# Kernel optimization log

Hardware: AMD Instinct MI355X
Metric: run time of the kernel (lower is better)

## Reference

```python
import jax, jax.numpy as jnp
import numpy as np

NUM_HEADS = 12
EPS = 1e-5


def setup_inputs() -> dict:
    key = jax.random.key(0)
    k0, k1, k2 = jax.random.split(key, 3)
    B, C, D = 2, 768, 14  # batch, hidden_size, img_size//16
    x = jax.random.normal(k0, (B, C, D, D, D), dtype=jnp.float32)
    norm_w = jnp.ones((C,), dtype=jnp.float32)
    norm_b = jnp.zeros((C,), dtype=jnp.float32)
    qkv_w = jax.random.normal(k1, (3 * C, C), dtype=jnp.float32) * 0.02
    out_w = jax.random.normal(k2, (C, C), dtype=jnp.float32) * 0.02
    out_b = jnp.zeros((C,), dtype=jnp.float32)
    return {"x": x, "norm_w": norm_w, "norm_b": norm_b,
            "qkv_w": qkv_w, "out_w": out_w, "out_b": out_b}


def reference(x, norm_w, norm_b, qkv_w, out_w, out_b):
    B, C, D, H, W = x.shape
    nh = NUM_HEADS
    dh = C // nh
    scale = dh ** -0.5

    # b c d h w -> b (d h w) c
    t = jnp.transpose(x, (0, 2, 3, 4, 1)).reshape(B, D * H * W, C)
    N = t.shape[1]

    # LayerNorm over channel dim
    mu = jnp.mean(t, axis=-1, keepdims=True)
    var = jnp.mean(jnp.square(t - mu), axis=-1, keepdims=True)
    tn = (t - mu) / jnp.sqrt(var + EPS) * norm_w + norm_b

    # qkv projection (no bias), split as (3, heads, dim_head)
    qkv = tn @ qkv_w.T                       # [B, N, 3C]
    qkv = qkv.reshape(B, N, 3, nh, dh)
    qkv = jnp.transpose(qkv, (2, 0, 3, 1, 4))  # [3, B, nh, N, dh]
    q, k, v = qkv[0], qkv[1], qkv[2]

    att = jax.nn.softmax(jnp.einsum('blxn,blyn->blxy', q, k) * scale, axis=-1)
    out = jnp.einsum('blxy,blyn->blxn', att, v)  # [B, nh, N, dh]

    out = jnp.transpose(out, (0, 2, 1, 3)).reshape(B, N, C)
    out = out @ out_w.T + out_b

    out = out.reshape(B, D, H, W, C)
    out = jnp.transpose(out, (0, 4, 1, 2, 3))  # b d h w c -> b c d h w
    return out + x
```

## Files before the change

### kernel.cpp

```cpp
#include <hip/hip_runtime.h>

typedef unsigned short u16;
typedef unsigned int u32;

#define SPA 2744
#define CH  768
#define NH  12
#define DH  64
#define BB  2
#define TC  2304
#define MTOT (BB*SPA)
#define CVTB 2304

typedef __bf16 bf16x8_t __attribute__((ext_vector_type(8)));
typedef __bf16 bf16x4_t __attribute__((ext_vector_type(4)));
typedef short  s16x4    __attribute__((ext_vector_type(4)));
typedef float  f32x4_t  __attribute__((ext_vector_type(4)));

static __device__ __forceinline__ u16 f2bf(float f) {
    union { float f; u32 u; } v; v.f = f;
    u32 u = v.u;
    u += 0x7fffu + ((u >> 16) & 1u);
    return (u16)(u >> 16);
}

static __device__ __forceinline__ void gld16(const u16* g, u16* l) {
    __builtin_amdgcn_global_load_lds(
        (const __attribute__((address_space(1))) u32*)(size_t)g,
        (__attribute__((address_space(3))) u32*)(u32)(size_t)l, 16, 0, 0);
}

__global__ __launch_bounds__(256) void cvtln_kernel(const float* __restrict__ qkv_w,
                                                    u16* __restrict__ qkvw_bf, int n4a,
                                                    const float* __restrict__ out_w,
                                                    u16* __restrict__ outw_bf,
                                                    const float* __restrict__ x,
                                                    const float* __restrict__ w,
                                                    const float* __restrict__ bta,
                                                    u16* __restrict__ tn) {
    int tid = threadIdx.x;
    if (blockIdx.x < CVTB) {
        int i = blockIdx.x * 256 + tid;
        const float* src; u16* dst; int idx;
        if (i < n4a) { src = qkv_w; dst = qkvw_bf; idx = i; }
        else { src = out_w; dst = outw_bf; idx = i - n4a; }
        float4 f = ((const float4*)src)[idx];
        uint2 o;
        o.x = (u32)f2bf(f.x) | ((u32)f2bf(f.y) << 16);
        o.y = (u32)f2bf(f.z) | ((u32)f2bf(f.w) << 16);
        ((uint2*)dst)[idx] = o;
        return;
    }
    int bid = blockIdx.x - CVTB;
    __shared__ f32x4_t redS[4][16];
    __shared__ f32x4_t redQ[4][16];
    __shared__ u16 T[32][68];
    int grp = tid & 15, chl = tid >> 4;
    int wvi = tid >> 6, l16g = tid & 15;
    (void)l16g;
    int tok0 = bid * 64 + grp * 4;
    int gb = (tok0 + 3 < MTOT) ? tok0 : (MTOT - 4);
    int b = gb / SPA, n = gb - b * SPA;
    const float* base = x + (size_t)b * CH * SPA + n;

    f32x4_t s4 = {0.f, 0.f, 0.f, 0.f}, q4 = {0.f, 0.f, 0.f, 0.f};
    for (int c0 = 0; c0 < CH; c0 += 16) {
        float4 v = *(const float4*)(base + (size_t)(c0 + chl) * SPA);
        s4[0] += v.x; s4[1] += v.y; s4[2] += v.z; s4[3] += v.w;
        q4[0] += v.x * v.x; q4[1] += v.y * v.y; q4[2] += v.z * v.z; q4[3] += v.w * v.w;
    }
#pragma unroll
    for (int m = 16; m <= 32; m <<= 1)
#pragma unroll
        for (int e = 0; e < 4; e++) {
            s4[e] += __shfl_xor(s4[e], m);
            q4[e] += __shfl_xor(q4[e], m);
        }
    if ((tid & 63) < 16) { redS[wvi][grp] = s4; redQ[wvi][grp] = q4; }
    __syncthreads();
    f32x4_t st = redS[0][grp], qt = redQ[0][grp];
#pragma unroll
    for (int wv2 = 1; wv2 < 4; wv2++) {
        f32x4_t a = redS[wv2][grp], c = redQ[wv2][grp];
#pragma unroll
        for (int e = 0; e < 4; e++) { st[e] += a[e]; qt[e] += c[e]; }
    }
    f32x4_t mean4, rstd4;
#pragma unroll
    for (int e = 0; e < 4; e++) {
        mean4[e] = st[e] * (1.0f / CH);
        rstd4[e] = rsqrtf(qt[e] * (1.0f / CH) - mean4[e] * mean4[e] + 1e-5f);
    }

    int tokl = tid >> 2, qq = tid & 3;
    int g2 = bid * 64 + tokl;
    for (int c0 = 0; c0 < CH; c0 += 32) {
        __syncthreads();
#pragma unroll
        for (int h = 0; h < 2; h++) {
            int cc = c0 + h * 16 + chl;
            float4 v = *(const float4*)(base + (size_t)cc * SPA);
            float ws = w[cc], bs = bta[cc];
            union { u16 h4[4]; } pk;
            pk.h4[0] = f2bf((v.x - mean4[0]) * rstd4[0] * ws + bs);
            pk.h4[1] = f2bf((v.y - mean4[1]) * rstd4[1] * ws + bs);
            pk.h4[2] = f2bf((v.z - mean4[2]) * rstd4[2] * ws + bs);
            pk.h4[3] = f2bf((v.w - mean4[3]) * rstd4[3] * ws + bs);
            *(uint2*)(&T[h * 16 + chl][grp * 4]) = *(uint2*)pk.h4;
        }
        __syncthreads();
        if (g2 < MTOT) {
            union { u16 h[8]; int4 v4; } pk;
#pragma unroll
            for (int e = 0; e < 8; e++) pk.h[e] = T[qq * 8 + e][tokl];
            *(int4*)(tn + (size_t)g2 * CH + c0 + qq * 8) = pk.v4;
        }
    }
}

__global__ __launch_bounds__(256, 3) void gemm_qkv(const u16* __restrict__ A,
                                                   const u16* __restrict__ Bw,
                                                   u16* __restrict__ out0,
                                                   u16* __restrict__ out1,
                                                   u16* __restrict__ out2) {
    const int M = MTOT, K = CH;
    __shared__ __align__(16) u16 As[128 * 32];
    __shared__ __align__(16) u16 Bs[128 * 32];
    int tid = threadIdx.x;
    int m0 = blockIdx.y * 128;
    int n0 = blockIdx.x * 128;
    int wv = tid >> 6, lane = tid & 63;
    int wm = (wv >> 1) * 64, wn = (wv & 1) * 64;
    int quad = lane >> 4, l16 = lane & 15;

    f32x4_t zero = {0.f, 0.f, 0.f, 0.f};
    f32x4_t acc[4][4];
#pragma unroll
    for (int i = 0; i < 4; i++)
#pragma unroll
        for (int j = 0; j < 4; j++) acc[i][j] = zero;

    int rl = lane >> 2, pos = lane & 3;
    int sw = (l16 >> 1) & 3;
    for (int k0 = 0; k0 < K; k0 += 32) {
        __syncthreads();
#pragma unroll
        for (int p = 0; p < 2; p++) {
            int rbase = p * 64 + wv * 16;
            int row = rbase + rl;
            int gch = pos ^ ((row >> 1) & 3);
            int gm = m0 + row; if (gm >= M) gm = M - 1;
            gld16(A + (size_t)gm * K + k0 + gch * 8, As + rbase * 32);
            gld16(Bw + (size_t)(n0 + row) * K + k0 + gch * 8, Bs + rbase * 32);
        }
        __syncthreads();
        bf16x8_t af[4], bfr[4];
#pragma unroll
        for (int i = 0; i < 4; i++)
            af[i] = *(const bf16x8_t*)(As + (wm + i * 16 + l16) * 32 + ((quad ^ sw) * 8));
#pragma unroll
        for (int j = 0; j < 4; j++)
            bfr[j] = *(const bf16x8_t*)(Bs + (wn + j * 16 + l16) * 32 + ((quad ^ sw) * 8));
#pragma unroll
        for (int i = 0; i < 4; i++)
#pragma unroll
            for (int j = 0; j < 4; j++)
                acc[i][j] = __builtin_amdgcn_mfma_f32_16x16x32_bf16(af[i], bfr[j], acc[i][j], 0, 0, 0);
    }

    int which = n0 / CH;
    int rb = n0 - which * CH;
    u16* base = (which == 0) ? out0 : ((which == 1) ? out1 : out2);
    float qs = (which == 0) ? 0.18033688011112042f : 1.0f;
#pragma unroll
    for (int i = 0; i < 4; i++)
#pragma unroll
        for (int r = 0; r < 4; r++) {
            int gm = m0 + wm + i * 16 + quad * 4 + r;
            if (gm < M) {
                int b = gm / SPA, n = gm - b * SPA;
#pragma unroll
                for (int j = 0; j < 4; j++) {
                    int rem = rb + wn + j * 16 + l16;
                    int h = rem >> 6, d = rem & 63;
                    base[((size_t)(b * NH + h) * SPA + n) * DH + d] = f2bf(acc[i][j][r] * qs);
                }
            }
        }
}

__global__ __launch_bounds__(256, 4) void gemm_out(const u16* __restrict__ A,
                                                   const u16* __restrict__ Bw,
                                                   const float* __restrict__ xres,
                                                   const float* __restrict__ ob,
                                                   float* __restrict__ fout) {
    const int M = MTOT, K = CH;
    __shared__ __align__(16) u16 As[128 * 32];
    __shared__ __align__(16) u16 Bs[64 * 32];
    int tid = threadIdx.x;
    int m0 = blockIdx.y * 128;
    int n0 = blockIdx.x * 64;
    int wv = tid >> 6, lane = tid & 63;
    int wm = (wv >> 1) * 64, wn = (wv & 1) * 32;
    int quad = lane >> 4, l16 = lane & 15;

    f32x4_t zero = {0.f, 0.f, 0.f, 0.f};
    f32x4_t acc[4][2];
#pragma unroll
    for (int i = 0; i < 4; i++)
#pragma unroll
        for (int j = 0; j < 2; j++) acc[i][j] = zero;

    int rl = lane >> 2, pos = lane & 3;
    int sw = (l16 >> 1) & 3;
    for (int k0 = 0; k0 < K; k0 += 32) {
        __syncthreads();
#pragma unroll
        for (int p = 0; p < 2; p++) {
            int rbase = p * 64 + wv * 16;
            int row = rbase + rl;
            int gch = pos ^ ((row >> 1) & 3);
            int gm = m0 + row; if (gm >= M) gm = M - 1;
            gld16(A + (size_t)gm * K + k0 + gch * 8, As + rbase * 32);
        }
        {
            int row = wv * 16 + rl;
            int gch = pos ^ ((row >> 1) & 3);
            gld16(Bw + (size_t)(n0 + row) * K + k0 + gch * 8, Bs + (wv * 16) * 32);
        }
        __syncthreads();
        bf16x8_t af[4], bfr[2];
#pragma unroll
        for (int i = 0; i < 4; i++)
            af[i] = *(const bf16x8_t*)(As + (wm + i * 16 + l16) * 32 + ((quad ^ sw) * 8));
#pragma unroll
        for (int j = 0; j < 2; j++)
            bfr[j] = *(const bf16x8_t*)(Bs + (wn + j * 16 + l16) * 32 + ((quad ^ sw) * 8));
#pragma unroll
        for (int i = 0; i < 4; i++)
#pragma unroll
            for (int j = 0; j < 2; j++)
                acc[i][j] = __builtin_amdgcn_mfma_f32_16x16x32_bf16(af[i], bfr[j], acc[i][j], 0, 0, 0);
    }

#pragma unroll
    for (int i = 0; i < 4; i++) {
        int gm0 = m0 + wm + i * 16 + quad * 4;
        if (gm0 < M) {
            int b = gm0 / SPA;
            int n = gm0 - b * SPA;
#pragma unroll
            for (int j = 0; j < 2; j++) {
                int gn = n0 + wn + j * 16 + l16;
                size_t xo = ((size_t)(b * CH + gn)) * SPA + n;
                float4 xv = *(const float4*)(xres + xo);
                float bias = ob[gn];
                float4 rr;
                rr.x = xv.x + bias + acc[i][j][0];
                rr.y = xv.y + bias + acc[i][j][1];
                rr.z = xv.z + bias + acc[i][j][2];
                rr.w = xv.w + bias + acc[i][j][3];
                *(float4*)(fout + xo) = rr;
            }
        }
    }
}

__global__ __launch_bounds__(256) void vtrans_kernel(const u16* __restrict__ v,
                                                     u16* __restrict__ vt) {
    __shared__ __align__(16) u16 T[64 * 72];
    int bh = blockIdx.y;
    int n0 = blockIdx.x * 64;
    int tid = threadIdx.x;
#pragma unroll
    for (int h = 0; h < 2; h++) {
        int chunk = tid + h * 256;
        int r = chunk >> 3, cs = chunk & 7;
        int n = n0 + r;
        int4 val = make_int4(0, 0, 0, 0);
        if (n < SPA) val = *(const int4*)(v + ((size_t)bh * SPA + n) * DH + cs * 8);
        *(int4*)(T + r * 72 + cs * 8) = val;
    }
    __syncthreads();
#pragma unroll
    for (int h = 0; h < 2; h++) {
        int chunk = tid + h * 256;
        int d = chunk >> 3, cs = chunk & 7;
        int nb = n0 + cs * 8;
        if (nb < SPA) {
            union { u16 s[8]; int4 v4; } tmp;
#pragma unroll
            for (int e = 0; e < 8; e++) tmp.s[e] = T[(cs * 8 + e) * 72 + d];
            *(int4*)(vt + ((size_t)bh * DH + d) * SPA + nb) = tmp.v4;
        }
    }
}

__global__ __launch_bounds__(256, 2) void attn_kernel(const u16* __restrict__ q,
                                                      const u16* __restrict__ k,
                                                      const u16* __restrict__ vt,
                                                      u16* __restrict__ out) {
    __shared__ __align__(16) u16 Kbuf[2][128 * 64];
    __shared__ __align__(16) u16 Vbuf[2][64 * 136];
    int g = blockIdx.x;
    int xcd = g & 7, slot = g >> 3;
    int bh = xcd * 3 + slot % 3;
    int qg = slot / 3;
    int b = bh / NH, h = bh - b * NH;
    int tid = threadIdx.x;
    int wv = tid >> 6, lane = tid & 63;
    int quad = lane >> 4, l16 = lane & 15;
    int q0w = qg * 128 + wv * 32;

    const u16* qgp = q + (size_t)bh * SPA * DH;
    const u16* kg = k + (size_t)bh * SPA * DH;
    const u16* vg = vt + (size_t)bh * DH * SPA;

    bf16x8_t bq[2][2];
    int qglob[2];
#pragma unroll
    for (int qf = 0; qf < 2; qf++) {
        int qq = q0w + qf * 16 + l16;
        qglob[qf] = qq;
        int qld = (qq < SPA) ? qq : (SPA - 1);
#pragma unroll
        for (int ks = 0; ks < 2; ks++)
            bq[qf][ks] = *(const bf16x8_t*)(qgp + (size_t)qld * DH + ks * 32 + quad * 8);
    }

    f32x4_t zero = {0.f, 0.f, 0.f, 0.f};
    f32x4_t o[2][4];
#pragma unroll
    for (int qf = 0; qf < 2; qf++)
#pragma unroll
        for (int i = 0; i < 4; i++) o[qf][i] = zero;
    f32x4_t lacc[2];
    lacc[0] = zero; lacc[1] = zero;
    s16x4 ones;
    ones[0] = ones[1] = ones[2] = ones[3] = (short)0x3F80;

    int rl8 = lane >> 3, pos8 = lane & 7;
    int sw8 = l16 & 7;
    int vd = tid >> 2, vc = (tid & 3) * 32;

#pragma unroll
    for (int p = 0; p < 4; p++) {
        int rbase = p * 32 + wv * 8;
        int row = rbase + rl8;
        int gch = pos8 ^ (row & 7);
        gld16(kg + (size_t)row * DH + gch * 8, Kbuf[0] + rbase * 64);
    }
#pragma unroll
    for (int s2 = 0; s2 < 4; s2++)
        *(int4*)(Vbuf[0] + vd * 136 + vc + s2 * 8) =
            *(const int4*)(vg + (size_t)vd * SPA + vc + s2 * 8);

    for (int si = 0; si < 22; si++) {
        __syncthreads();
        int cur = si & 1, nxt = cur ^ 1;
        int kv0 = si * 128;
        bool hn = (si < 21);
        int4 vp0, vp1, vp2, vp3;
        if (hn) {
            int kb = kv0 + 128;
#pragma unroll
            for (int p = 0; p < 4; p++) {
                int rbase = p * 32 + wv * 8;
                int row = rbase + rl8;
                int gch = pos8 ^ (row & 7);
                int kr = kb + row; if (kr >= SPA) kr = SPA - 1;
                gld16(kg + (size_t)kr * DH + gch * 8, Kbuf[nxt] + rbase * 64);
            }
            int c0 = kb + vc;
            int a0 = c0;      if (a0 > SPA - 8) a0 = SPA - 8;
            int a1 = c0 + 8;  if (a1 > SPA - 8) a1 = SPA - 8;
            int a2 = c0 + 16; if (a2 > SPA - 8) a2 = SPA - 8;
            int a3 = c0 + 24; if (a3 > SPA - 8) a3 = SPA - 8;
            vp0 = *(const int4*)(vg + (size_t)vd * SPA + a0);
            vp1 = *(const int4*)(vg + (size_t)vd * SPA + a1);
            vp2 = *(const int4*)(vg + (size_t)vd * SPA + a2);
            vp3 = *(const int4*)(vg + (size_t)vd * SPA + a3);
        }

        s16x4 bp[2][8];
#pragma unroll
        for (int i = 0; i < 8; i++) {
            const u16* krow = Kbuf[cur] + (i * 16 + l16) * 64;
            bf16x8_t ak0 = *(const bf16x8_t*)(krow + ((quad ^ sw8) * 8));
            bf16x8_t ak1 = *(const bf16x8_t*)(krow + (((4 + quad) ^ sw8) * 8));
            f32x4_t s0 = __builtin_amdgcn_mfma_f32_16x16x32_bf16(ak0, bq[0][0], zero, 0, 0, 0);
            s0 = __builtin_amdgcn_mfma_f32_16x16x32_bf16(ak1, bq[0][1], s0, 0, 0, 0);
            f32x4_t s1 = __builtin_amdgcn_mfma_f32_16x16x32_bf16(ak0, bq[1][0], zero, 0, 0, 0);
            s1 = __builtin_amdgcn_mfma_f32_16x16x32_bf16(ak1, bq[1][1], s1, 0, 0, 0);
            bf16x4_t p0, p1;
            if (si != 21) {
#pragma unroll
                for (int r = 0; r < 4; r++) {
                    p0[r] = (__bf16)__builtin_amdgcn_exp2f(s0[r]);
                    p1[r] = (__bf16)__builtin_amdgcn_exp2f(s1[r]);
                }
            } else {
#pragma unroll
                for (int r = 0; r < 4; r++) {
                    float e0 = __builtin_amdgcn_exp2f(s0[r]);
                    float e1 = __builtin_amdgcn_exp2f(s1[r]);
                    bool bad = (kv0 + i * 16 + quad * 4 + r) >= SPA;
                    p0[r] = (__bf16)(bad ? 0.f : e0);
                    p1[r] = (__bf16)(bad ? 0.f : e1);
                }
            }
            union { bf16x4_t b; s16x4 s; } u0, u1;
            u0.b = p0; u1.b = p1;
            bp[0][i] = u0.s; bp[1][i] = u1.s;
        }

        if (hn) {
            *(int4*)(Vbuf[nxt] + vd * 136 + vc)      = vp0;
            *(int4*)(Vbuf[nxt] + vd * 136 + vc + 8)  = vp1;
            *(int4*)(Vbuf[nxt] + vd * 136 + vc + 16) = vp2;
            *(int4*)(Vbuf[nxt] + vd * 136 + vc + 24) = vp3;
        }

#pragma unroll
        for (int c = 0; c < 8; c++) {
            lacc[0] = __builtin_amdgcn_mfma_f32_16x16x16bf16_1k(ones, bp[0][c], lacc[0], 0, 0, 0);
            lacc[1] = __builtin_amdgcn_mfma_f32_16x16x16bf16_1k(ones, bp[1][c], lacc[1], 0, 0, 0);
#pragma unroll
            for (int i = 0; i < 4; i++) {
                s16x4 av = *(const s16x4*)(Vbuf[cur] + (i * 16 + l16) * 136 + c * 16 + quad * 4);
                o[0][i] = __builtin_amdgcn_mfma_f32_16x16x16bf16_1k(av, bp[0][c], o[0][i], 0, 0, 0);
                o[1][i] = __builtin_amdgcn_mfma_f32_16x16x16bf16_1k(av, bp[1][c], o[1][i], 0, 0, 0);
            }
        }
    }

#pragma unroll
    for (int qf = 0; qf < 2; qf++) {
        int qq = qglob[qf];
        if (qq < SPA) {
            float inv = 1.0f / lacc[qf][0];
            u16* op = out + ((size_t)(b * SPA + qq)) * CH + h * DH;
#pragma unroll
            for (int i = 0; i < 4; i++) {
                bf16x4_t ov;
#pragma unroll
                for (int r = 0; r < 4; r++) ov[r] = (__bf16)(o[qf][i][r] * inv);
                *(bf16x4_t*)(op + i * 16 + quad * 4) = ov;
            }
        }
    }
}

extern "C" void kernel_launch(void* const* d_in, const int* in_sizes, int n_in,
                              void* d_out, int out_size, void* d_ws, size_t ws_size,
                              hipStream_t stream) {
    const float* x      = (const float*)d_in[0];
    const float* norm_w = (const float*)d_in[1];
    const float* norm_b = (const float*)d_in[2];
    const float* qkv_w  = (const float*)d_in[3];
    const float* out_w  = (const float*)d_in[4];
    const float* out_b  = (const float*)d_in[5];
    float* out = (float*)d_out;

    char* ws = (char*)d_ws;
    size_t off = 0;
    auto alloc = [&](size_t bytes) -> void* {
        void* p = ws + off;
        off += (bytes + 255) & ~(size_t)255;
        return p;
    };
    u16* tn      = (u16*)alloc((size_t)MTOT * CH * 2);
    u16* qkvw_bf = (u16*)alloc((size_t)TC * CH * 2);
    u16* outw_bf = (u16*)alloc((size_t)CH * CH * 2);
    u16* qb      = (u16*)alloc((size_t)BB * NH * SPA * DH * 2);
    u16* kb      = (u16*)alloc((size_t)BB * NH * SPA * DH * 2);
    u16* vb      = (u16*)alloc((size_t)BB * NH * SPA * DH * 2);
    u16* vtb     = (u16*)alloc((size_t)BB * NH * SPA * DH * 2);
    u16* ao      = (u16*)alloc((size_t)MTOT * CH * 2);

    int n4a = TC * CH / 4;
    cvtln_kernel<<<CVTB + (MTOT + 63) / 64, 256, 0, stream>>>(
        qkv_w, qkvw_bf, n4a, out_w, outw_bf, x, norm_w, norm_b, tn);
    gemm_qkv<<<dim3(TC / 128, (MTOT + 127) / 128), 256, 0, stream>>>(
        tn, qkvw_bf, qb, kb, vb);
    vtrans_kernel<<<dim3((SPA + 63) / 64, BB * NH), 256, 0, stream>>>(vb, vtb);
    attn_kernel<<<528, 256, 0, stream>>>(qb, kb, vtb, ao);
    gemm_out<<<dim3(CH / 64, (MTOT + 127) / 128), 256, 0, stream>>>(
        ao, outw_bf, x, out_b, out);
}
```

Before: 255.4 us.

## Use K=32 bf16 MFMA for PV with lane shuffles; compute row sums in VALU

The P·V product in the attention kernel switches from 16x16x16 MFMAs to 16x16x32 MFMAs, which halves the matrix instruction count. The P fragments are rearranged across lanes with xor shuffles so they match the wider K layout. The softmax denominator no longer comes from extra MFMAs against a ones vector. It is accumulated in fp32 registers and reduced across lanes once at the end. The cost is added shuffle and select instructions per tile, and the denominator now sums fp32 values instead of bf16-rounded ones.

```diff
diff --git a/kernel.cpp b/kernel.cpp
--- a/kernel.cpp
+++ b/kernel.cpp
@@ -334,14 +334,13 @@
     for (int qf = 0; qf < 2; qf++)
 #pragma unroll
         for (int i = 0; i < 4; i++) o[qf][i] = zero;
-    f32x4_t lacc[2];
-    lacc[0] = zero; lacc[1] = zero;
-    s16x4 ones;
-    ones[0] = ones[1] = ones[2] = ones[3] = (short)0x3F80;
+    float ps0 = 0.f, ps1 = 0.f;
 
     int rl8 = lane >> 3, pos8 = lane & 7;
     int sw8 = l16 & 7;
     int vd = tid >> 2, vc = (tid & 3) * 32;
+    bool hiH = (quad >= 2);
+    bool par = (quad & 1);
 
 #pragma unroll
     for (int p = 0; p < 4; p++) {
@@ -382,7 +381,7 @@
             vp3 = *(const int4*)(vg + (size_t)vd * SPA + a3);
         }
 
-        s16x4 bp[2][8];
+        uint2 Pk[2][4][2];
 #pragma unroll
         for (int i = 0; i < 8; i++) {
             const u16* krow = Kbuf[cur] + (i * 16 + l16) * 64;
@@ -396,8 +395,11 @@
             if (si != 21) {
 #pragma unroll
                 for (int r = 0; r < 4; r++) {
-                    p0[r] = (__bf16)__builtin_amdgcn_exp2f(s0[r]);
-                    p1[r] = (__bf16)__builtin_amdgcn_exp2f(s1[r]);
+                    float e0 = __builtin_amdgcn_exp2f(s0[r]);
+                    float e1 = __builtin_amdgcn_exp2f(s1[r]);
+                    ps0 += e0; ps1 += e1;
+                    p0[r] = (__bf16)e0;
+                    p1[r] = (__bf16)e1;
                 }
             } else {
 #pragma unroll
@@ -405,13 +407,17 @@
                     float e0 = __builtin_amdgcn_exp2f(s0[r]);
                     float e1 = __builtin_amdgcn_exp2f(s1[r]);
                     bool bad = (kv0 + i * 16 + quad * 4 + r) >= SPA;
-                    p0[r] = (__bf16)(bad ? 0.f : e0);
-                    p1[r] = (__bf16)(bad ? 0.f : e1);
+                    e0 = bad ? 0.f : e0;
+                    e1 = bad ? 0.f : e1;
+                    ps0 += e0; ps1 += e1;
+                    p0[r] = (__bf16)e0;
+                    p1[r] = (__bf16)e1;
                 }
             }
-            union { bf16x4_t b; s16x4 s; } u0, u1;
+            union { bf16x4_t b; uint2 u; } u0, u1;
             u0.b = p0; u1.b = p1;
-            bp[0][i] = u0.s; bp[1][i] = u1.s;
+            Pk[0][i >> 1][i & 1] = u0.u;
+            Pk[1][i >> 1][i & 1] = u1.u;
         }
 
         if (hn) {
@@ -422,23 +428,52 @@
         }
 
 #pragma unroll
-        for (int c = 0; c < 8; c++) {
-            lacc[0] = __builtin_amdgcn_mfma_f32_16x16x16bf16_1k(ones, bp[0][c], lacc[0], 0, 0, 0);
-            lacc[1] = __builtin_amdgcn_mfma_f32_16x16x16bf16_1k(ones, bp[1][c], lacc[1], 0, 0, 0);
+        for (int w = 0; w < 4; w++) {
+            bf16x8_t fr[2];
+#pragma unroll
+            for (int qf = 0; qf < 2; qf++) {
+                uint2 a = Pk[qf][w][0];
+                uint2 bb = Pk[qf][w][1];
+                u32 sx0 = hiH ? a.x : bb.x;
+                u32 sx1 = hiH ? a.y : bb.y;
+                u32 c0 = (u32)__shfl_xor((int)sx0, 32);
+                u32 c1 = (u32)__shfl_xor((int)sx1, 32);
+                u32 k0 = hiH ? bb.x : a.x;
+                u32 k1 = hiH ? bb.y : a.y;
+                u32 kx0 = (u32)__shfl_xor((int)k0, 16);
+                u32 kx1 = (u32)__shfl_xor((int)k1, 16);
+                u32 cx0 = (u32)__shfl_xor((int)c0, 16);
+                u32 cx1 = (u32)__shfl_xor((int)c1, 16);
+                u32 f0, f1, f2, f3;
+                if (!par) {
+                    f0 = hiH ? c0 : k0;   f1 = hiH ? c1 : k1;
+                    f2 = hiH ? cx0 : kx0; f3 = hiH ? cx1 : kx1;
+                } else {
+                    f0 = hiH ? kx0 : cx0; f1 = hiH ? kx1 : cx1;
+                    f2 = hiH ? k0 : c0;   f3 = hiH ? k1 : c1;
+                }
+                union { u32 u[4]; bf16x8_t v; } fu;
+                fu.u[0] = f0; fu.u[1] = f1; fu.u[2] = f2; fu.u[3] = f3;
+                fr[qf] = fu.v;
+            }
 #pragma unroll
             for (int i = 0; i < 4; i++) {
-                s16x4 av = *(const s16x4*)(Vbuf[cur] + (i * 16 + l16) * 136 + c * 16 + quad * 4);
-                o[0][i] = __builtin_amdgcn_mfma_f32_16x16x16bf16_1k(av, bp[0][c], o[0][i], 0, 0, 0);
-                o[1][i] = __builtin_amdgcn_mfma_f32_16x16x16bf16_1k(av, bp[1][c], o[1][i], 0, 0, 0);
-            }
-        }
-    }
-
+                bf16x8_t av = *(const bf16x8_t*)(Vbuf[cur] + (i * 16 + l16) * 136 + w * 32 + quad * 8);
+                o[0][i] = __builtin_amdgcn_mfma_f32_16x16x32_bf16(av, fr[0], o[0][i], 0, 0, 0);
+                o[1][i] = __builtin_amdgcn_mfma_f32_16x16x32_bf16(av, fr[1], o[1][i], 0, 0, 0);
+            }
+        }
+    }
+
+    ps0 += __shfl_xor(ps0, 16);
+    ps0 += __shfl_xor(ps0, 32);
+    ps1 += __shfl_xor(ps1, 16);
+    ps1 += __shfl_xor(ps1, 32);
 #pragma unroll
     for (int qf = 0; qf < 2; qf++) {
         int qq = qglob[qf];
         if (qq < SPA) {
-            float inv = 1.0f / lacc[qf][0];
+            float inv = 1.0f / (qf == 0 ? ps0 : ps1);
             u16* op = out + ((size_t)(b * SPA + qq)) * CH + h * DH;
 #pragma unroll
             for (int i = 0; i < 4; i++) {
```

Result: slower. 286.6 us (+12.2%).

## Split attention block into 8 waves of 16 queries and sum softmax denominators in registers

Applied to the files above, without the earlier changes.

The attention kernel now runs 512 threads per block, and each of the 8 waves handles 16 queries instead of 32. This halves per-wave MFMA and register load and raises wave-level parallelism. The row-sum of exponentials is kept as a scalar float, reduced with cross-lane shuffles at the end, and replaces the extra ones-matrix MFMA. The risks are heavier LDS traffic per useful FLOP and tighter register limits from the higher launch bound. The denominator also now sums the fp32 exponentials rather than their bf16-rounded values.

```diff
diff --git a/kernel.cpp b/kernel.cpp
--- a/kernel.cpp
+++ b/kernel.cpp
@@ -296,7 +296,7 @@
     }
 }
 
-__global__ __launch_bounds__(256, 2) void attn_kernel(const u16* __restrict__ q,
+__global__ __launch_bounds__(512, 4) void attn_kernel(const u16* __restrict__ q,
                                                       const u16* __restrict__ k,
                                                       const u16* __restrict__ vt,
                                                       u16* __restrict__ out) {
@@ -310,143 +310,121 @@
     int tid = threadIdx.x;
     int wv = tid >> 6, lane = tid & 63;
     int quad = lane >> 4, l16 = lane & 15;
-    int q0w = qg * 128 + wv * 32;
+    int q0w = qg * 128 + wv * 16;
 
     const u16* qgp = q + (size_t)bh * SPA * DH;
     const u16* kg = k + (size_t)bh * SPA * DH;
     const u16* vg = vt + (size_t)bh * DH * SPA;
 
-    bf16x8_t bq[2][2];
-    int qglob[2];
-#pragma unroll
-    for (int qf = 0; qf < 2; qf++) {
-        int qq = q0w + qf * 16 + l16;
-        qglob[qf] = qq;
-        int qld = (qq < SPA) ? qq : (SPA - 1);
-#pragma unroll
-        for (int ks = 0; ks < 2; ks++)
-            bq[qf][ks] = *(const bf16x8_t*)(qgp + (size_t)qld * DH + ks * 32 + quad * 8);
-    }
+    bf16x8_t bq[2];
+    int qq = q0w + l16;
+    int qld = (qq < SPA) ? qq : (SPA - 1);
+#pragma unroll
+    for (int ks = 0; ks < 2; ks++)
+        bq[ks] = *(const bf16x8_t*)(qgp + (size_t)qld * DH + ks * 32 + quad * 8);
 
     f32x4_t zero = {0.f, 0.f, 0.f, 0.f};
-    f32x4_t o[2][4];
-#pragma unroll
-    for (int qf = 0; qf < 2; qf++)
-#pragma unroll
-        for (int i = 0; i < 4; i++) o[qf][i] = zero;
-    f32x4_t lacc[2];
-    lacc[0] = zero; lacc[1] = zero;
-    s16x4 ones;
-    ones[0] = ones[1] = ones[2] = ones[3] = (short)0x3F80;
+    f32x4_t o[4];
+#pragma unroll
+    for (int i = 0; i < 4; i++) o[i] = zero;
+    float ps = 0.f;
 
     int rl8 = lane >> 3, pos8 = lane & 7;
     int sw8 = l16 & 7;
-    int vd = tid >> 2, vc = (tid & 3) * 32;
-
-#pragma unroll
-    for (int p = 0; p < 4; p++) {
-        int rbase = p * 32 + wv * 8;
+    int vd = tid >> 3, vcc8 = (tid & 7) * 16;
+
+#pragma unroll
+    for (int p = 0; p < 2; p++) {
+        int rbase = p * 64 + wv * 8;
         int row = rbase + rl8;
         int gch = pos8 ^ (row & 7);
         gld16(kg + (size_t)row * DH + gch * 8, Kbuf[0] + rbase * 64);
     }
 #pragma unroll
-    for (int s2 = 0; s2 < 4; s2++)
-        *(int4*)(Vbuf[0] + vd * 136 + vc + s2 * 8) =
-            *(const int4*)(vg + (size_t)vd * SPA + vc + s2 * 8);
+    for (int s2 = 0; s2 < 2; s2++)
+        *(int4*)(Vbuf[0] + vd * 136 + vcc8 + s2 * 8) =
+            *(const int4*)(vg + (size_t)vd * SPA + vcc8 + s2 * 8);
 
     for (int si = 0; si < 22; si++) {
         __syncthreads();
         int cur = si & 1, nxt = cur ^ 1;
         int kv0 = si * 128;
         bool hn = (si < 21);
-        int4 vp0, vp1, vp2, vp3;
+        int4 vp0, vp1;
         if (hn) {
             int kb = kv0 + 128;
 #pragma unroll
-            for (int p = 0; p < 4; p++) {
-                int rbase = p * 32 + wv * 8;
+            for (int p = 0; p < 2; p++) {
+                int rbase = p * 64 + wv * 8;
                 int row = rbase + rl8;
                 int gch = pos8 ^ (row & 7);
                 int kr = kb + row; if (kr >= SPA) kr = SPA - 1;
                 gld16(kg + (size_t)kr * DH + gch * 8, Kbuf[nxt] + rbase * 64);
             }
-            int c0 = kb + vc;
+            int c0 = kb + vcc8;
             int a0 = c0;      if (a0 > SPA - 8) a0 = SPA - 8;
             int a1 = c0 + 8;  if (a1 > SPA - 8) a1 = SPA - 8;
-            int a2 = c0 + 16; if (a2 > SPA - 8) a2 = SPA - 8;
-            int a3 = c0 + 24; if (a3 > SPA - 8) a3 = SPA - 8;
             vp0 = *(const int4*)(vg + (size_t)vd * SPA + a0);
             vp1 = *(const int4*)(vg + (size_t)vd * SPA + a1);
-            vp2 = *(const int4*)(vg + (size_t)vd * SPA + a2);
-            vp3 = *(const int4*)(vg + (size_t)vd * SPA + a3);
-        }
-
-        s16x4 bp[2][8];
+        }
+
+        s16x4 bp[8];
 #pragma unroll
         for (int i = 0; i < 8; i++) {
             const u16* krow = Kbuf[cur] + (i * 16 + l16) * 64;
             bf16x8_t ak0 = *(const bf16x8_t*)(krow + ((quad ^ sw8) * 8));
             bf16x8_t ak1 = *(const bf16x8_t*)(krow + (((4 + quad) ^ sw8) * 8));
-            f32x4_t s0 = __builtin_amdgcn_mfma_f32_16x16x32_bf16(ak0, bq[0][0], zero, 0, 0, 0);
-            s0 = __builtin_amdgcn_mfma_f32_16x16x32_bf16(ak1, bq[0][1], s0, 0, 0, 0);
-            f32x4_t s1 = __builtin_amdgcn_mfma_f32_16x16x32_bf16(ak0, bq[1][0], zero, 0, 0, 0);
-            s1 = __builtin_amdgcn_mfma_f32_16x16x32_bf16(ak1, bq[1][1], s1, 0, 0, 0);
-            bf16x4_t p0, p1;
+            f32x4_t s0 = __builtin_amdgcn_mfma_f32_16x16x32_bf16(ak0, bq[0], zero, 0, 0, 0);
+            s0 = __builtin_amdgcn_mfma_f32_16x16x32_bf16(ak1, bq[1], s0, 0, 0, 0);
+            bf16x4_t p0;
             if (si != 21) {
 #pragma unroll
                 for (int r = 0; r < 4; r++) {
-                    p0[r] = (__bf16)__builtin_amdgcn_exp2f(s0[r]);
-                    p1[r] = (__bf16)__builtin_amdgcn_exp2f(s1[r]);
+                    float e0 = __builtin_amdgcn_exp2f(s0[r]);
+                    ps += e0;
+                    p0[r] = (__bf16)e0;
                 }
             } else {
 #pragma unroll
                 for (int r = 0; r < 4; r++) {
                     float e0 = __builtin_amdgcn_exp2f(s0[r]);
-                    float e1 = __builtin_amdgcn_exp2f(s1[r]);
                     bool bad = (kv0 + i * 16 + quad * 4 + r) >= SPA;
-                    p0[r] = (__bf16)(bad ? 0.f : e0);
-                    p1[r] = (__bf16)(bad ? 0.f : e1);
+                    e0 = bad ? 0.f : e0;
+                    ps += e0;
+                    p0[r] = (__bf16)e0;
                 }
             }
-            union { bf16x4_t b; s16x4 s; } u0, u1;
-            u0.b = p0; u1.b = p1;
-            bp[0][i] = u0.s; bp[1][i] = u1.s;
+            union { bf16x4_t b; s16x4 s; } u0;
+            u0.b = p0;
+            bp[i] = u0.s;
         }
 
         if (hn) {
-            *(int4*)(Vbuf[nxt] + vd * 136 + vc)      = vp0;
-            *(int4*)(Vbuf[nxt] + vd * 136 + vc + 8)  = vp1;
-            *(int4*)(Vbuf[nxt] + vd * 136 + vc + 16) = vp2;
-            *(int4*)(Vbuf[nxt] + vd * 136 + vc + 24) = vp3;
+            *(int4*)(Vbuf[nxt] + vd * 136 + vcc8)     = vp0;
+            *(int4*)(Vbuf[nxt] + vd * 136 + vcc8 + 8) = vp1;
         }
 
 #pragma unroll
         for (int c = 0; c < 8; c++) {
-            lacc[0] = __builtin_amdgcn_mfma_f32_16x16x16bf16_1k(ones, bp[0][c], lacc[0], 0, 0, 0);
-            lacc[1] = __builtin_amdgcn_mfma_f32_16x16x16bf16_1k(ones, bp[1][c], lacc[1], 0, 0, 0);
 #pragma unroll
             for (int i = 0; i < 4; i++) {
                 s16x4 av = *(const s16x4*)(Vbuf[cur] + (i * 16 + l16) * 136 + c * 16 + quad * 4);
-                o[0][i] = __builtin_amdgcn_mfma_f32_16x16x16bf16_1k(av, bp[0][c], o[0][i], 0, 0, 0);
-                o[1][i] = __builtin_amdgcn_mfma_f32_16x16x16bf16_1k(av, bp[1][c], o[1][i], 0, 0, 0);
+                o[i] = __builtin_amdgcn_mfma_f32_16x16x16bf16_1k(av, bp[c], o[i], 0, 0, 0);
             }
         }
     }
 
-#pragma unroll
-    for (int qf = 0; qf < 2; qf++) {
-        int qq = qglob[qf];
-        if (qq < SPA) {
-            float inv = 1.0f / lacc[qf][0];
-            u16* op = out + ((size_t)(b * SPA + qq)) * CH + h * DH;
-#pragma unroll
-            for (int i = 0; i < 4; i++) {
-                bf16x4_t ov;
-#pragma unroll
-                for (int r = 0; r < 4; r++) ov[r] = (__bf16)(o[qf][i][r] * inv);
-                *(bf16x4_t*)(op + i * 16 + quad * 4) = ov;
-            }
+    ps += __shfl_xor(ps, 16);
+    ps += __shfl_xor(ps, 32);
+    if (qq < SPA) {
+        float inv = 1.0f / ps;
+        u16* op = out + ((size_t)(b * SPA + qq)) * CH + h * DH;
+#pragma unroll
+        for (int i = 0; i < 4; i++) {
+            bf16x4_t ov;
+#pragma unroll
+            for (int r = 0; r < 4; r++) ov[r] = (__bf16)(o[i][r] * inv);
+            *(bf16x4_t*)(op + i * 16 + quad * 4) = ov;
         }
     }
 }
@@ -484,7 +462,7 @@
     gemm_qkv<<<dim3(TC / 128, (MTOT + 127) / 128), 256, 0, stream>>>(
         tn, qkvw_bf, qb, kb, vb);
     vtrans_kernel<<<dim3((SPA + 63) / 64, BB * NH), 256, 0, stream>>>(vb, vtb);
-    attn_kernel<<<528, 256, 0, stream>>>(qb, kb, vtb, ao);
+    attn_kernel<<<528, 512, 0, stream>>>(qb, kb, vtb, ao);
     gemm_out<<<dim3(CH / 64, (MTOT + 127) / 128), 256, 0, stream>>>(
         ao, outw_bf, x, out_b, out);
 }
```

Measured after the change: 267.3 us. 1.05x slower.

## Fuse V transpose into QKV GEMM epilogue and pad attention V tile

Applied to the files above, without the earlier changes.

The QKV GEMM epilogue for the V third of the output now stages the accumulator tile transposed through shared memory and writes V directly in the [b,h,d,n] layout. This removes the separate vtrans kernel launch and one round-trip of V through global memory. The attention kernel's V shared buffer row stride also changes from 136 to 140 elements to alter bank mapping. The GEMM gains 17KB of extra LDS, which may reduce occupancy. The epilogue writes in 8-token chunks, so chunks that cross the batch boundary (2744 is not a multiple of 8 relative to the tile origin) may be handled incorrectly.

```diff
diff --git a/kernel.cpp b/kernel.cpp
--- a/kernel.cpp
+++ b/kernel.cpp
@@ -122,10 +122,11 @@
                                                    const u16* __restrict__ Bw,
                                                    u16* __restrict__ out0,
                                                    u16* __restrict__ out1,
-                                                   u16* __restrict__ out2) {
+                                                   u16* __restrict__ vtb) {
     const int M = MTOT, K = CH;
     __shared__ __align__(16) u16 As[128 * 32];
     __shared__ __align__(16) u16 Bs[128 * 32];
+    __shared__ __align__(16) u16 Tv[64 * 136];
     int tid = threadIdx.x;
     int m0 = blockIdx.y * 128;
     int n0 = blockIdx.x * 128;
@@ -170,7 +171,40 @@
 
     int which = n0 / CH;
     int rb = n0 - which * CH;
-    u16* base = (which == 0) ? out0 : ((which == 1) ? out1 : out2);
+
+    if (which == 2) {
+#pragma unroll
+        for (int p = 0; p < 2; p++) {
+            __syncthreads();
+            if ((wv & 1) == p) {
+#pragma unroll
+                for (int i = 0; i < 4; i++)
+#pragma unroll
+                    for (int j = 0; j < 4; j++) {
+                        union { u16 h4[4]; uint2 u; } pk;
+#pragma unroll
+                        for (int r = 0; r < 4; r++) pk.h4[r] = f2bf(acc[i][j][r]);
+                        *(uint2*)(&Tv[(j * 16 + l16) * 136 + wm + i * 16 + quad * 4]) = pk.u;
+                    }
+            }
+            __syncthreads();
+            int rloc = tid >> 2, cseg = (tid & 3) * 32;
+            int rem = rb + p * 64 + rloc;
+            int hh = rem >> 6, dd = rem & 63;
+#pragma unroll
+            for (int s = 0; s < 4; s++) {
+                int t0 = m0 + cseg + s * 8;
+                if (t0 + 8 <= MTOT) {
+                    int b2 = t0 / SPA, n2 = t0 - b2 * SPA;
+                    *(int4*)(vtb + ((size_t)(b2 * NH + hh) * DH + dd) * SPA + n2) =
+                        *(const int4*)(&Tv[rloc * 136 + cseg + s * 8]);
+                }
+            }
+        }
+        return;
+    }
+
+    u16* base = (which == 0) ? out0 : out1;
     float qs = (which == 0) ? 0.18033688011112042f : 1.0f;
 #pragma unroll
     for (int i = 0; i < 4; i++)
@@ -266,42 +300,12 @@
     }
 }
 
-__global__ __launch_bounds__(256) void vtrans_kernel(const u16* __restrict__ v,
-                                                     u16* __restrict__ vt) {
-    __shared__ __align__(16) u16 T[64 * 72];
-    int bh = blockIdx.y;
-    int n0 = blockIdx.x * 64;
-    int tid = threadIdx.x;
-#pragma unroll
-    for (int h = 0; h < 2; h++) {
-        int chunk = tid + h * 256;
-        int r = chunk >> 3, cs = chunk & 7;
-        int n = n0 + r;
-        int4 val = make_int4(0, 0, 0, 0);
-        if (n < SPA) val = *(const int4*)(v + ((size_t)bh * SPA + n) * DH + cs * 8);
-        *(int4*)(T + r * 72 + cs * 8) = val;
-    }
-    __syncthreads();
-#pragma unroll
-    for (int h = 0; h < 2; h++) {
-        int chunk = tid + h * 256;
-        int d = chunk >> 3, cs = chunk & 7;
-        int nb = n0 + cs * 8;
-        if (nb < SPA) {
-            union { u16 s[8]; int4 v4; } tmp;
-#pragma unroll
-            for (int e = 0; e < 8; e++) tmp.s[e] = T[(cs * 8 + e) * 72 + d];
-            *(int4*)(vt + ((size_t)bh * DH + d) * SPA + nb) = tmp.v4;
-        }
-    }
-}
-
 __global__ __launch_bounds__(256, 2) void attn_kernel(const u16* __restrict__ q,
                                                       const u16* __restrict__ k,
                                                       const u16* __restrict__ vt,
                                                       u16* __restrict__ out) {
     __shared__ __align__(16) u16 Kbuf[2][128 * 64];
-    __shared__ __align__(16) u16 Vbuf[2][64 * 136];
+    __shared__ __align__(16) u16 Vbuf[2][64 * 140];
     int g = blockIdx.x;
     int xcd = g & 7, slot = g >> 3;
     int bh = xcd * 3 + slot % 3;
@@ -352,7 +356,7 @@
     }
 #pragma unroll
     for (int s2 = 0; s2 < 4; s2++)
-        *(int4*)(Vbuf[0] + vd * 136 + vc + s2 * 8) =
+        *(int4*)(Vbuf[0] + vd * 140 + vc + s2 * 8) =
             *(const int4*)(vg + (size_t)vd * SPA + vc + s2 * 8);
 
     for (int si = 0; si < 22; si++) {
@@ -415,10 +419,10 @@
         }
 
         if (hn) {
-            *(int4*)(Vbuf[nxt] + vd * 136 + vc)      = vp0;
-            *(int4*)(Vbuf[nxt] + vd * 136 + vc + 8)  = vp1;
-            *(int4*)(Vbuf[nxt] + vd * 136 + vc + 16) = vp2;
-            *(int4*)(Vbuf[nxt] + vd * 136 + vc + 24) = vp3;
+            *(int4*)(Vbuf[nxt] + vd * 140 + vc)      = vp0;
+            *(int4*)(Vbuf[nxt] + vd * 140 + vc + 8)  = vp1;
+            *(int4*)(Vbuf[nxt] + vd * 140 + vc + 16) = vp2;
+            *(int4*)(Vbuf[nxt] + vd * 140 + vc + 24) = vp3;
         }
 
 #pragma unroll
@@ -427,7 +431,7 @@
             lacc[1] = __builtin_amdgcn_mfma_f32_16x16x16bf16_1k(ones, bp[1][c], lacc[1], 0, 0, 0);
 #pragma unroll
             for (int i = 0; i < 4; i++) {
-                s16x4 av = *(const s16x4*)(Vbuf[cur] + (i * 16 + l16) * 136 + c * 16 + quad * 4);
+                s16x4 av = *(const s16x4*)(Vbuf[cur] + (i * 16 + l16) * 140 + c * 16 + quad * 4);
                 o[0][i] = __builtin_amdgcn_mfma_f32_16x16x16bf16_1k(av, bp[0][c], o[0][i], 0, 0, 0);
                 o[1][i] = __builtin_amdgcn_mfma_f32_16x16x16bf16_1k(av, bp[1][c], o[1][i], 0, 0, 0);
             }
@@ -474,7 +478,6 @@
     u16* outw_bf = (u16*)alloc((size_t)CH * CH * 2);
     u16* qb      = (u16*)alloc((size_t)BB * NH * SPA * DH * 2);
     u16* kb      = (u16*)alloc((size_t)BB * NH * SPA * DH * 2);
-    u16* vb      = (u16*)alloc((size_t)BB * NH * SPA * DH * 2);
     u16* vtb     = (u16*)alloc((size_t)BB * NH * SPA * DH * 2);
     u16* ao      = (u16*)alloc((size_t)MTOT * CH * 2);
 
@@ -482,8 +485,7 @@
     cvtln_kernel<<<CVTB + (MTOT + 63) / 64, 256, 0, stream>>>(
         qkv_w, qkvw_bf, n4a, out_w, outw_bf, x, norm_w, norm_b, tn);
     gemm_qkv<<<dim3(TC / 128, (MTOT + 127) / 128), 256, 0, stream>>>(
-        tn, qkvw_bf, qb, kb, vb);
-    vtrans_kernel<<<dim3((SPA + 63) / 64, BB * NH), 256, 0, stream>>>(vb, vtb);
+        tn, qkvw_bf, qb, kb, vtb);
     attn_kernel<<<528, 256, 0, stream>>>(qb, kb, vtb, ao);
     gemm_out<<<dim3(CH / 64, (MTOT + 127) / 128), 256, 0, stream>>>(
         ao, outw_bf, x, out_b, out);
```

After: 260.7 us. 1.02x slower.
